# Kernel optimization log

Measured on AMD Instinct MI355X. Metric: run time of the kernel, lower is better.

The kernel has to match this reference:

```python
import jax, jax.numpy as jnp
import numpy as np

N = 50000
IN_CH = 128
OUT_CH = 64
HEADS = 4
NEG_SLOPE = 0.2


def _gatv2(x, src, dst, W_l, W_r, att):
    """GATv2Conv, concat=False, no bias/residual/dropout.
    x: [N, in]; src/dst: [E]; W_l/W_r: [in, H*C]; att: [H, C].
    Returns [N, C] (mean over heads)."""
    n = x.shape[0]
    xl = (x @ W_l).reshape(n, HEADS, OUT_CH)
    xr = (x @ W_r).reshape(n, HEADS, OUT_CH)
    # per-edge message: x_j (source, lin_l) + x_i (target, lin_r)
    m = jax.nn.leaky_relu(xl[src] + xr[dst], negative_slope=NEG_SLOPE)  # [E,H,C]
    e = jnp.einsum('ehc,hc->eh', m, att)  # [E,H]
    # segment softmax over incoming edges of each dst node
    emax = jax.ops.segment_max(e, dst, num_segments=n)  # [N,H] (-inf for empty)
    ex = jnp.exp(e - emax[dst])
    denom = jax.ops.segment_sum(ex, dst, num_segments=n)  # [N,H]
    alpha = ex / denom[dst]
    out = jax.ops.segment_sum(alpha[:, :, None] * xl[src], dst, num_segments=n)  # [N,H,C]
    return out.mean(axis=1)


def setup_inputs() -> dict:
    key = jax.random.key(0)
    ks = jax.random.split(key, 9)
    E = 800000
    s = 1.0 / np.sqrt(IN_CH)
    return {
        'x': jax.random.normal(ks[0], (N, IN_CH), dtype=jnp.float32),
        'edge_index1': jax.random.randint(ks[1], (2, E), 0, N, dtype=jnp.int64),
        'edge_index2': jax.random.randint(ks[2], (2, E), 0, N, dtype=jnp.int64),
        'W_l': jax.random.normal(ks[3], (IN_CH, HEADS * OUT_CH), dtype=jnp.float32) * s,  # shared lin_l
        'W_r0': jax.random.normal(ks[4], (IN_CH, HEADS * OUT_CH), dtype=jnp.float32) * s,
        'W_r1': jax.random.normal(ks[5], (IN_CH, HEADS * OUT_CH), dtype=jnp.float32) * s,
        'att0': jax.random.normal(ks[6], (HEADS, OUT_CH), dtype=jnp.float32) * (1.0 / np.sqrt(OUT_CH)),
        'att1': jax.random.normal(ks[7], (HEADS, OUT_CH), dtype=jnp.float32) * (1.0 / np.sqrt(OUT_CH)),
        'theta': jnp.zeros((1,), dtype=jnp.float32),
    }


def reference(x, edge_index1, edge_index2, W_l, W_r0, W_r1, att0, att1, theta):
    n = x.shape[0]
    # hop 0: add self loops
    loop = jnp.arange(n, dtype=edge_index1.dtype)
    src0 = jnp.concatenate([edge_index1[0], loop])
    dst0 = jnp.concatenate([edge_index1[1], loop])
    out = _gatv2(x, src0, dst0, W_l, W_r0, att0)
    # hop 1: no self loops, gated residual sum
    out = out + jax.nn.sigmoid(theta[0]) * _gatv2(x, edge_index2[0], edge_index2[1], W_l, W_r1, att1)
    return out
```

## Files before the change

kernel.cpp:

```cpp
#include <hip/hip_runtime.h>
#include <hip/hip_bf16.h>
#include <math.h>

#define IN_CH   128
#define HC      256
#define OUT_C   64

typedef unsigned short ushort_t;
typedef __attribute__((ext_vector_type(2))) float v2f;
typedef __attribute__((ext_vector_type(4))) float v4f;
typedef __attribute__((ext_vector_type(8))) short bf16x8;

__device__ __forceinline__ ushort_t f2bf_rne(float f) {
    unsigned u = __float_as_uint(f);
    unsigned r = (u + 0x7FFFu + ((u >> 16) & 1u)) >> 16;
    return (ushort_t)r;
}
__device__ __forceinline__ v2f bfpair(unsigned u) {
    v2f r;
    r.x = __uint_as_float(u << 16);
    r.y = __uint_as_float(u & 0xffff0000u);
    return r;
}
__device__ __forceinline__ v2f vmax0(v2f a) {
    v2f r;
    r.x = fmaxf(a.x, 0.f);
    r.y = fmaxf(a.y, 0.f);
    return r;
}

__device__ __forceinline__ float4 ntld4(const float* p) {
    v4f t = __builtin_nontemporal_load((const v4f*)p);
    return make_float4(t.x, t.y, t.z, t.w);
}
__device__ __forceinline__ int ntldi(const int* p) {
    return __builtin_nontemporal_load(p);
}
__device__ __forceinline__ void ntst4(float* p, float4 v) {
    v4f t = {v.x, v.y, v.z, v.w};
    __builtin_nontemporal_store(t, (v4f*)p);
}
__device__ __forceinline__ void ntsti(int* p, int v) {
    __builtin_nontemporal_store(v, p);
}

#define DPP_ROR_ADD(x, N)                                                   \
    (x) += __uint_as_float(__builtin_amdgcn_update_dpp(                     \
        0, __float_as_uint(x), 0x120 + (N), 0xF, 0xF, true))

__device__ __forceinline__ float rowsum16(float x) {
    DPP_ROR_ADD(x, 8);
    DPP_ROR_ADD(x, 4);
    DPP_ROR_ADD(x, 2);
    DPP_ROR_ADD(x, 1);
    return x;
}

__device__ __forceinline__ bf16x8 ldbf(const uint4* p) {
    union { uint4 u; bf16x8 v; } t;
    t.u = *p;
    return t.v;
}

__device__ __forceinline__ void dev_gemm(const float* __restrict__ x,
                                         const float* __restrict__ W,
                                         float* __restrict__ outf,
                                         ushort_t* __restrict__ outh,
                                         int n, int bx) {
    const int tid = threadIdx.x;
    const int c4  = tid & 63;
    const int rg  = __builtin_amdgcn_readfirstlane(tid >> 6);
    const int row0 = bx * 64 + rg * 16;
    const int nm1 = n - 1;
    const float4* Wv = (const float4*)W;
    const float* xr[16];
#pragma unroll
    for (int j = 0; j < 16; ++j) {
        int r = row0 + j;
        xr[j] = x + (size_t)(r > nm1 ? nm1 : r) * IN_CH;
    }
    v2f acc[16][2];
#pragma unroll
    for (int j = 0; j < 16; ++j) {
        acc[j][0] = (v2f){0.f, 0.f};
        acc[j][1] = (v2f){0.f, 0.f};
    }
    for (int k = 0; k < IN_CH; k += 4) {
        const float4 w0 = Wv[(k + 0) * 64 + c4];
        const float4 w1 = Wv[(k + 1) * 64 + c4];
        const float4 w2 = Wv[(k + 2) * 64 + c4];
        const float4 w3 = Wv[(k + 3) * 64 + c4];
        const v2f w0a = {w0.x, w0.y}, w0b = {w0.z, w0.w};
        const v2f w1a = {w1.x, w1.y}, w1b = {w1.z, w1.w};
        const v2f w2a = {w2.x, w2.y}, w2b = {w2.z, w2.w};
        const v2f w3a = {w3.x, w3.y}, w3b = {w3.z, w3.w};
#pragma unroll
        for (int jb = 0; jb < 2; ++jb) {
            float4 xv[8];
#pragma unroll
            for (int j = 0; j < 8; ++j) xv[j] = *(const float4*)(xr[jb * 8 + j] + k);
#pragma unroll
            for (int j = 0; j < 8; ++j) {
                const int a = jb * 8 + j;
                const v2f s0 = {xv[j].x, xv[j].x}, s1 = {xv[j].y, xv[j].y};
                const v2f s2 = {xv[j].z, xv[j].z}, s3 = {xv[j].w, xv[j].w};
                acc[a][0] = s0 * w0a + acc[a][0];
                acc[a][1] = s0 * w0b + acc[a][1];
                acc[a][0] = s1 * w1a + acc[a][0];
                acc[a][1] = s1 * w1b + acc[a][1];
                acc[a][0] = s2 * w2a + acc[a][0];
                acc[a][1] = s2 * w2b + acc[a][1];
                acc[a][0] = s3 * w3a + acc[a][0];
                acc[a][1] = s3 * w3b + acc[a][1];
            }
        }
    }
#pragma unroll
    for (int j = 0; j < 16; ++j) {
        const int row = row0 + j;
        if (row < n) {
            if (outh) {
                ushort4 h;
                h.x = f2bf_rne(acc[j][0].x);
                h.y = f2bf_rne(acc[j][0].y);
                h.z = f2bf_rne(acc[j][1].x);
                h.w = f2bf_rne(acc[j][1].y);
                ((ushort4*)(outh + (size_t)row * HC))[c4] = h;
            } else {
                ntst4(outf + (size_t)row * HC + 4 * c4,
                      make_float4(acc[j][0].x, acc[j][0].y, acc[j][1].x, acc[j][1].y));
            }
        }
    }
}

__device__ __forceinline__ void dev_scatter_rank(const int* __restrict__ src1,
                                                 const int* __restrict__ dst1, int E1,
                                                 const int* __restrict__ src2,
                                                 const int* __restrict__ dst2, int E2,
                                                 int n, const int* __restrict__ offs,
                                                 const int* __restrict__ rank,
                                                 int* __restrict__ csr,
                                                 int bid, int nB) {
    const int Et = E1 + E2;
    for (int i = bid * 256 + threadIdx.x; i < Et; i += nB * 256) {
        if (i < E1) {
            csr[offs[ntldi(dst1 + i)] + ntldi(rank + i)] = ntldi(src1 + i) << 9;
        } else {
            int j = i - E1;
            csr[offs[n + ntldi(dst2 + j)] + ntldi(rank + i)] = ntldi(src2 + j) << 9;
        }
    }
}

__global__ __launch_bounds__(256) void k_hp(const float* __restrict__ x,
                                            const float* __restrict__ Wl,
                                            const float* __restrict__ Wr0,
                                            const float* __restrict__ Wr1,
                                            uint4* __restrict__ xAh,
                                            uint4* __restrict__ xAl,
                                            uint4* __restrict__ WBh,
                                            uint4* __restrict__ WBl,
                                            int n, int GH, int gPX,
                                            const int* __restrict__ dst1, int E1,
                                            const int* __restrict__ dst2, int E2,
                                            int* __restrict__ deg,
                                            int* __restrict__ rank) {
    const int bx = blockIdx.x;
    if (bx < GH) {
        const int Et = E1 + E2;
        for (int i = bx * 256 + threadIdx.x; i < Et; i += GH * 256) {
            if (i < E1) ntsti(rank + i, atomicAdd(&deg[ntldi(dst1 + i)], 1));
            else        ntsti(rank + i, atomicAdd(&deg[n + ntldi(dst2 + i - E1)], 1));
        }
        return;
    }
    const int t = bx - GH;
    float v[8];
    ushort_t h[8], l[8];
    if (t < gPX) {
        const int di  = t * 256 + threadIdx.x;
        const int row = ((di >> 8) << 4) | (di & 15);
        const int ko  = ((di >> 4) & 3) | (((di >> 6) & 3) << 2);
        float4 v0 = make_float4(0.f, 0.f, 0.f, 0.f), v1 = v0;
        if (row < n) {
            const float4* xp = (const float4*)(x + (size_t)row * IN_CH + ko * 8);
            v0 = xp[0];
            v1 = xp[1];
        }
        v[0] = v0.x; v[1] = v0.y; v[2] = v0.z; v[3] = v0.w;
        v[4] = v1.x; v[5] = v1.y; v[6] = v1.z; v[7] = v1.w;
#pragma unroll
        for (int j = 0; j < 8; ++j) {
            h[j] = f2bf_rne(v[j]);
            l[j] = f2bf_rne(v[j] - __uint_as_float((unsigned)h[j] << 16));
        }
        uint4 ph, pl;
        ph.x = (unsigned)h[0] | ((unsigned)h[1] << 16);
        ph.y = (unsigned)h[2] | ((unsigned)h[3] << 16);
        ph.z = (unsigned)h[4] | ((unsigned)h[5] << 16);
        ph.w = (unsigned)h[6] | ((unsigned)h[7] << 16);
        pl.x = (unsigned)l[0] | ((unsigned)l[1] << 16);
        pl.y = (unsigned)l[2] | ((unsigned)l[3] << 16);
        pl.z = (unsigned)l[4] | ((unsigned)l[5] << 16);
        pl.w = (unsigned)l[6] | ((unsigned)l[7] << 16);
        xAh[di] = ph;
        xAl[di] = pl;
    } else {
        const int idx = (t - gPX) * 256 + threadIdx.x;
        const int lane = idx & 63;
        const int f    = (idx >> 6) & 15;
        const int c    = (idx >> 10) & 3;
        const int w    = idx >> 12;
        if (w >= 3) return;
        const float* Wp = (w == 0) ? Wl : ((w == 1) ? Wr0 : Wr1);
        const int col = f * 16 + (lane & 15);
        const int k0  = c * 32 + (lane >> 4) * 8;
#pragma unroll
        for (int j = 0; j < 8; ++j) {
            v[j] = Wp[(size_t)(k0 + j) * HC + col];
            h[j] = f2bf_rne(v[j]);
            l[j] = f2bf_rne(v[j] - __uint_as_float((unsigned)h[j] << 16));
        }
        uint4 ph, pl;
        ph.x = (unsigned)h[0] | ((unsigned)h[1] << 16);
        ph.y = (unsigned)h[2] | ((unsigned)h[3] << 16);
        ph.z = (unsigned)h[4] | ((unsigned)h[5] << 16);
        ph.w = (unsigned)h[6] | ((unsigned)h[7] << 16);
        pl.x = (unsigned)l[0] | ((unsigned)l[1] << 16);
        pl.y = (unsigned)l[2] | ((unsigned)l[3] << 16);
        pl.z = (unsigned)l[4] | ((unsigned)l[5] << 16);
        pl.w = (unsigned)l[6] | ((unsigned)l[7] << 16);
        WBh[idx] = ph;
        WBl[idx] = pl;
    }
}

__global__ __launch_bounds__(256) void k_gemm3(const uint4* __restrict__ xAh,
                                               const uint4* __restrict__ xAl,
                                               const uint4* __restrict__ WBh,
                                               const uint4* __restrict__ WBl,
                                               ushort_t* __restrict__ xlh,
                                               float* __restrict__ xr0,
                                               float* __restrict__ xr1,
                                               int n, int GS,
                                               const int* __restrict__ src1,
                                               const int* __restrict__ dst1, int E1,
                                               const int* __restrict__ src2,
                                               const int* __restrict__ dst2, int E2,
                                               const int* __restrict__ offs,
                                               const int* __restrict__ rank,
                                               int* __restrict__ csr) {
    const int bx = blockIdx.x;
    if (bx < GS) {
        dev_scatter_rank(src1, dst1, E1, src2, dst2, E2, n, offs, rank, csr, bx, GS);
        return;
    }
    const int t    = bx - GS;
    const int tile = t / 3;
    const int wsel = t - tile * 3;

    const int lane = threadIdx.x & 63;
    const int wave = __builtin_amdgcn_readfirstlane((int)(threadIdx.x >> 6));

    v4f acc[4][4];
#pragma unroll
    for (int g = 0; g < 4; ++g)
#pragma unroll
        for (int f = 0; f < 4; ++f) acc[g][f] = (v4f){0.f, 0.f, 0.f, 0.f};

    const uint4* Bh = WBh + (size_t)wsel * 4096;
    const uint4* Bl = WBl + (size_t)wsel * 4096;
    const int g0 = tile * 4;

    for (int c = 0; c < 4; ++c) {
        bf16x8 ah[4], al[4], bh[4], bl[4];
#pragma unroll
        for (int g = 0; g < 4; ++g) {
            const int ai = ((g0 + g) * 4 + c) * 64 + lane;
            ah[g] = ldbf(xAh + ai);
            al[g] = ldbf(xAl + ai);
        }
#pragma unroll
        for (int f = 0; f < 4; ++f) {
            const int bi = (c * 16 + wave * 4 + f) * 64 + lane;
            bh[f] = ldbf(Bh + bi);
            bl[f] = ldbf(Bl + bi);
        }
#pragma unroll
        for (int g = 0; g < 4; ++g)
#pragma unroll
            for (int f = 0; f < 4; ++f) {
                acc[g][f] = __builtin_amdgcn_mfma_f32_16x16x32_bf16(ah[g], bh[f], acc[g][f], 0, 0, 0);
                acc[g][f] = __builtin_amdgcn_mfma_f32_16x16x32_bf16(ah[g], bl[f], acc[g][f], 0, 0, 0);
                acc[g][f] = __builtin_amdgcn_mfma_f32_16x16x32_bf16(al[g], bh[f], acc[g][f], 0, 0, 0);
            }
    }

    const int colB = wave * 64 + (lane & 15);
    const int rowB = tile * 64 + ((lane >> 4) << 2);
    if (wsel == 0) {
#pragma unroll
        for (int g = 0; g < 4; ++g)
#pragma unroll
            for (int f = 0; f < 4; ++f) {
                const int col = colB + f * 16;
#pragma unroll
                for (int r = 0; r < 4; ++r) {
                    const int row = rowB + g * 16 + r;
                    if (row < n) xlh[(size_t)row * HC + col] = f2bf_rne(acc[g][f][r]);
                }
            }
    } else {
        float* o = (wsel == 1) ? xr0 : xr1;
#pragma unroll
        for (int g = 0; g < 4; ++g)
#pragma unroll
            for (int f = 0; f < 4; ++f) {
                const int col = colB + f * 16;
#pragma unroll
                for (int r = 0; r < 4; ++r) {
                    const int row = rowB + g * 16 + r;
                    if (row < n)
                        __builtin_nontemporal_store(acc[g][f][r], o + (size_t)row * HC + col);
                }
            }
    }
}

__global__ __launch_bounds__(128) void k_aggboth(const ushort_t* __restrict__ xlh,
                                                 const float* __restrict__ xr0,
                                                 const float* __restrict__ xr1,
                                                 const float* __restrict__ att0,
                                                 const float* __restrict__ att1,
                                                 const int* __restrict__ offs,
                                                 const int* __restrict__ deg,
                                                 const int* __restrict__ csr,
                                                 int n, float* __restrict__ out,
                                                 const float* __restrict__ theta) {
    const int lane = threadIdx.x & 63;
    int node_ = blockIdx.x * 2 + (threadIdx.x >> 6);
    if (node_ >= n) return;
    const int node = __builtin_amdgcn_readfirstlane(node_);

    const float4 at0 = ((const float4*)att0)[lane];
    const float4 at1 = ((const float4*)att1)[lane];
    const v2f a2_0a = {0.2f * at0.x, 0.2f * at0.y}, a2_0b = {0.2f * at0.z, 0.2f * at0.w};
    const v2f a8_0a = {0.8f * at0.x, 0.8f * at0.y}, a8_0b = {0.8f * at0.z, 0.8f * at0.w};
    const v2f a2_1a = {0.2f * at1.x, 0.2f * at1.y}, a2_1b = {0.2f * at1.z, 0.2f * at1.w};
    const v2f a8_1a = {0.8f * at1.x, 0.8f * at1.y}, a8_1b = {0.8f * at1.z, 0.8f * at1.w};
    const float4 q0 = ntld4(xr0 + (size_t)node * HC + 4 * lane);
    const float4 q1 = ntld4(xr1 + (size_t)node * HC + 4 * lane);
    const v2f x0a = {q0.x, q0.y}, x0b = {q0.z, q0.w};
    const v2f x1a = {q1.x, q1.y}, x1b = {q1.z, q1.w};

    const int t0 = deg[node];
    const int s0 = offs[node];
    const int t1 = deg[n + node];
    const int s1 = offs[n + node];

    const char* Xc = (const char*)xlh;
    const unsigned laneB = (unsigned)lane * 8u;
    auto gath = [&](unsigned off) -> uint2 {
        const char* p = Xc + off;
        return *(const uint2*)(p + laneB);
    };

    float l0 = 0.f, l1 = 0.f;
    v2f O0a = {0.f, 0.f}, O0b = {0.f, 0.f};
    v2f O1a = {0.f, 0.f}, O1b = {0.f, 0.f};

    auto proc = [&](uint2 w, const v2f& xa, const v2f& xb,
                    const v2f& a8a, const v2f& a8b,
                    const v2f& a2a, const v2f& a2b, float& l, v2f& Oa, v2f& Ob) {
        v2f ca = bfpair(w.x), cb = bfpair(w.y);
        v2f za = ca + xa, zb = cb + xb;
        v2f t = a2a * za + a2b * zb + a8a * vmax0(za) + a8b * vmax0(zb);
        float part = rowsum16(t.x + t.y);
        float p = __expf(fminf(part, 60.f));
        l += p;
        v2f pp = {p, p};
        Oa = pp * ca + Oa;
        Ob = pp * cb + Ob;
    };
    auto proc0 = [&](uint2 w) { proc(w, x0a, x0b, a8_0a, a8_0b, a2_0a, a2_0b, l0, O0a, O0b); };
    auto proc1 = [&](uint2 w) { proc(w, x1a, x1b, a8_1a, a8_1b, a2_1a, a2_1b, l1, O1a, O1b); };

    unsigned vc0p = 0, vc1p = 0;
    if (t0 > 0) vc0p = (unsigned)csr[s0 + lane];
    if (t1 > 0) vc1p = (unsigned)csr[s1 + lane];

    proc0(gath((unsigned)node << 9));

    for (int base = 0; base < t0; base += 64) {
        const unsigned vc = (base == 0) ? vc0p : (unsigned)csr[s0 + base + lane];
        const int m = (t0 - base < 64) ? (t0 - base) : 64;
        int j = 0;
        for (; j + 8 <= m; j += 8) {
            uint2 g0 = gath((unsigned)__builtin_amdgcn_readlane(vc, j + 0));
            uint2 g1 = gath((unsigned)__builtin_amdgcn_readlane(vc, j + 1));
            uint2 g2 = gath((unsigned)__builtin_amdgcn_readlane(vc, j + 2));
            uint2 g3 = gath((unsigned)__builtin_amdgcn_readlane(vc, j + 3));
            uint2 g4 = gath((unsigned)__builtin_amdgcn_readlane(vc, j + 4));
            uint2 g5 = gath((unsigned)__builtin_amdgcn_readlane(vc, j + 5));
            uint2 g6 = gath((unsigned)__builtin_amdgcn_readlane(vc, j + 6));
            uint2 g7 = gath((unsigned)__builtin_amdgcn_readlane(vc, j + 7));
            proc0(g0); proc0(g1); proc0(g2); proc0(g3);
            proc0(g4); proc0(g5); proc0(g6); proc0(g7);
        }
        for (; j + 2 <= m; j += 2) {
            uint2 g0 = gath((unsigned)__builtin_amdgcn_readlane(vc, j + 0));
            uint2 g1 = gath((unsigned)__builtin_amdgcn_readlane(vc, j + 1));
            proc0(g0); proc0(g1);
        }
        if (j < m) proc0(gath((unsigned)__builtin_amdgcn_readlane(vc, j)));
    }

    for (int base = 0; base < t1; base += 64) {
        const unsigned vc = (base == 0) ? vc1p : (unsigned)csr[s1 + base + lane];
        const int m = (t1 - base < 64) ? (t1 - base) : 64;
        int j = 0;
        for (; j + 8 <= m; j += 8) {
            uint2 g0 = gath((unsigned)__builtin_amdgcn_readlane(vc, j + 0));
            uint2 g1 = gath((unsigned)__builtin_amdgcn_readlane(vc, j + 1));
            uint2 g2 = gath((unsigned)__builtin_amdgcn_readlane(vc, j + 2));
            uint2 g3 = gath((unsigned)__builtin_amdgcn_readlane(vc, j + 3));
            uint2 g4 = gath((unsigned)__builtin_amdgcn_readlane(vc, j + 4));
            uint2 g5 = gath((unsigned)__builtin_amdgcn_readlane(vc, j + 5));
            uint2 g6 = gath((unsigned)__builtin_amdgcn_readlane(vc, j + 6));
            uint2 g7 = gath((unsigned)__builtin_amdgcn_readlane(vc, j + 7));
            proc1(g0); proc1(g1); proc1(g2); proc1(g3);
            proc1(g4); proc1(g5); proc1(g6); proc1(g7);
        }
        for (; j + 2 <= m; j += 2) {
            uint2 g0 = gath((unsigned)__builtin_amdgcn_readlane(vc, j + 0));
            uint2 g1 = gath((unsigned)__builtin_amdgcn_readlane(vc, j + 1));
            proc1(g0); proc1(g1);
        }
        if (j < m) proc1(gath((unsigned)__builtin_amdgcn_readlane(vc, j)));
    }

    const float inv0 = 0.25f / l0;
    const float inv1 = (l1 > 0.f) ? 0.25f / l1 : 0.f;
    const float sg = 1.f / (1.f + __expf(-theta[0]));
    float vx = O0a.x * inv0 + sg * (O1a.x * inv1);
    float vy = O0a.y * inv0 + sg * (O1a.y * inv1);
    float vz = O0b.x * inv0 + sg * (O1b.x * inv1);
    float vw = O0b.y * inv0 + sg * (O1b.y * inv1);
    vx += __shfl_xor(vx, 16); vx += __shfl_xor(vx, 32);
    vy += __shfl_xor(vy, 16); vy += __shfl_xor(vy, 32);
    vz += __shfl_xor(vz, 16); vz += __shfl_xor(vz, 32);
    vw += __shfl_xor(vw, 16); vw += __shfl_xor(vw, 32);

    if (lane < 16) {
        ntst4(out + (size_t)node * OUT_C + 4 * lane, make_float4(vx, vy, vz, vw));
    }
}

__device__ __forceinline__ void dev_agg(const ushort_t* __restrict__ xlh,
                                        const float* __restrict__ xr,
                                        const float* __restrict__ att,
                                        const int* __restrict__ offs,
                                        const int* __restrict__ deg,
                                        const int* __restrict__ csr_src,
                                        int n, float* __restrict__ out,
                                        int selfLoop,
                                        const float* __restrict__ theta,
                                        int accumulate, int bid) {
    const int lane = threadIdx.x & 63;
    const int node = bid * 4 + (threadIdx.x >> 6);
    if (node >= n) return;

    const float4 attv = ((const float4*)att)[lane];
    const v2f a2a = {0.2f * attv.x, 0.2f * attv.y}, a2b = {0.2f * attv.z, 0.2f * attv.w};
    const v2f a8a = {0.8f * attv.x, 0.8f * attv.y}, a8b = {0.8f * attv.z, 0.8f * attv.w};
    const float4 q = ntld4(xr + (size_t)node * HC + 4 * lane);
    const v2f xa = {q.x, q.y}, xb = {q.z, q.w};
    const int start2 = offs[node] - selfLoop;
    const int total  = deg[node] + selfLoop;

    float l = 0.f;
    v2f Oa = {0.f, 0.f}, Ob = {0.f, 0.f};
    const char* Xc = (const char*)xlh;
    const unsigned laneB = (unsigned)lane * 8u;

    auto ld = [&](int i) -> uint2 {
        int off = (selfLoop && i == 0) ? (node << 9) : ntldi(csr_src + start2 + i);
        return *(const uint2*)(Xc + (unsigned)off + laneB);
    };
    auto process = [&](uint2 w) {
        v2f ca = bfpair(w.x), cb = bfpair(w.y);
        v2f za = ca + xa, zb = cb + xb;
        v2f t = a2a * za + a2b * zb + a8a * vmax0(za) + a8b * vmax0(zb);
        float part = rowsum16(t.x + t.y);
        float p = __expf(fminf(part, 60.f));
        l += p;
        v2f pp = {p, p};
        Oa = pp * ca + Oa;
        Ob = pp * cb + Ob;
    };

    if (total > 0) {
        uint2 b0 = ld(0);
        uint2 b1 = ld(1);
        uint2 b2 = ld(2);
        uint2 b3 = ld(3);
        int i = 0;
        for (; i + 4 <= total; i += 4) {
            uint2 c0 = b0, c1 = b1, c2 = b2, c3 = b3;
            b0 = ld(i + 4);
            b1 = ld(i + 5);
            b2 = ld(i + 6);
            b3 = ld(i + 7);
            process(c0);
            process(c1);
            process(c2);
            process(c3);
        }
        const int rem = total - i;
        if (rem > 0) process(b0);
        if (rem > 1) process(b1);
        if (rem > 2) process(b2);
    }

    float inv = (l > 0.f) ? 0.25f / l : 0.f;
    float vx = Oa.x * inv, vy = Oa.y * inv, vz = Ob.x * inv, vw = Ob.y * inv;
    vx += __shfl_xor(vx, 16); vx += __shfl_xor(vx, 32);
    vy += __shfl_xor(vy, 16); vy += __shfl_xor(vy, 32);
    vz += __shfl_xor(vz, 16); vz += __shfl_xor(vz, 32);
    vw += __shfl_xor(vw, 16); vw += __shfl_xor(vw, 32);

    if (lane < 16) {
        float4 r = make_float4(vx, vy, vz, vw);
        float4* op = (float4*)(out + (size_t)node * OUT_C);
        if (accumulate) {
            float sg = 1.f / (1.f + __expf(-theta[0]));
            float4 cur = op[lane];
            r.x = fmaf(sg, r.x, cur.x);
            r.y = fmaf(sg, r.y, cur.y);
            r.z = fmaf(sg, r.z, cur.z);
            r.w = fmaf(sg, r.w, cur.w);
        }
        op[lane] = r;
    }
}

__global__ __launch_bounds__(256) void k_mix1(const float* __restrict__ x,
                                              const float* __restrict__ Wa,
                                              ushort_t* __restrict__ oah,
                                              const float* __restrict__ Wb,
                                              float* __restrict__ ob, int n,
                                              int GH, int gG,
                                              const int* __restrict__ dst1, int E1,
                                              const int* __restrict__ dst2, int E2,
                                              int* __restrict__ deg,
                                              int* __restrict__ rank) {
    const int bx = blockIdx.x;
    if (bx < GH) {
        const int Et = E1 + E2;
        for (int i = bx * 256 + threadIdx.x; i < Et; i += GH * 256) {
            if (i < E1) ntsti(rank + i, atomicAdd(&deg[ntldi(dst1 + i)], 1));
            else        ntsti(rank + i, atomicAdd(&deg[n + ntldi(dst2 + i - E1)], 1));
        }
    } else {
        int t = bx - GH;
        if (t < gG) dev_gemm(x, Wa, nullptr, oah, n, t);
        else        dev_gemm(x, Wb, ob, nullptr, n, t - gG);
    }
}

__global__ __launch_bounds__(256) void k_mix2(const float* __restrict__ x,
                                              const float* __restrict__ Wc,
                                              float* __restrict__ oc, int n,
                                              int GS,
                                              const int* __restrict__ src1,
                                              const int* __restrict__ dst1, int E1,
                                              const int* __restrict__ src2,
                                              const int* __restrict__ dst2, int E2,
                                              const int* __restrict__ offs,
                                              const int* __restrict__ rank,
                                              int* __restrict__ csr) {
    const int bx = blockIdx.x;
    if (bx < GS)
        dev_scatter_rank(src1, dst1, E1, src2, dst2, E2, n, offs, rank, csr, bx, GS);
    else
        dev_gemm(x, Wc, oc, nullptr, n, bx - GS);
}

__global__ __launch_bounds__(256) void k_mix3(const ushort_t* __restrict__ xlh,
                                              const float* __restrict__ xr,
                                              const float* __restrict__ att,
                                              const int* __restrict__ offs,
                                              const int* __restrict__ deg,
                                              const int* __restrict__ csr_src,
                                              int n, float* __restrict__ out,
                                              int selfLoop,
                                              const float* __restrict__ theta,
                                              int accumulate) {
    dev_agg(xlh, xr, att, offs, deg, csr_src, n, out, selfLoop, theta,
            accumulate, blockIdx.x);
}

__global__ __launch_bounds__(1024) void k_scanA(const int* __restrict__ deg, int n,
                                                int* __restrict__ incl,
                                                int* __restrict__ bsum) {
    __shared__ int sm[1024];
    const int t = threadIdx.x;
    const int i = blockIdx.x * 1024 + t;
    sm[t] = (i < n) ? deg[i] : 0;
    for (int off = 1; off < 1024; off <<= 1) {
        __syncthreads();
        int u = (t >= off) ? sm[t - off] : 0;
        __syncthreads();
        sm[t] += u;
    }
    if (i < n) incl[i] = sm[t];
    if (t == 1023) bsum[blockIdx.x] = sm[1023];
}

__global__ __launch_bounds__(1024) void k_scanB(int* __restrict__ bsum, int nb) {
    __shared__ int sm[1024];
    const int t = threadIdx.x;
    sm[t] = (t < nb) ? bsum[t] : 0;
    for (int off = 1; off < 1024; off <<= 1) {
        __syncthreads();
        int u = (t >= off) ? sm[t - off] : 0;
        __syncthreads();
        sm[t] += u;
    }
    if (t < nb) bsum[t] = sm[t];
}

__global__ void k_scanCf(const int* __restrict__ incl, const int* __restrict__ deg,
                         const int* __restrict__ bsum, int nb, int n,
                         int* __restrict__ offs) {
    __shared__ int sb[128];
    const int t = threadIdx.x;
    if (t < 128) sb[t] = (t < nb) ? bsum[t] : 0;
    __syncthreads();
#pragma unroll
    for (int off = 1; off < 128; off <<= 1) {
        int u = (t >= off && t < 128) ? sb[t - off] : 0;
        __syncthreads();
        if (t < 128) sb[t] += u;
        __syncthreads();
    }
    int i = blockIdx.x * 256 + t;
    if (i < n) {
        int b    = i >> 10;
        int base = (b > 0) ? sb[b - 1] : 0;
        offs[i] = base + incl[i] - deg[i];
    }
}

__global__ void k_scanC(const int* __restrict__ incl, const int* __restrict__ deg,
                        const int* __restrict__ bsum, int n,
                        int* __restrict__ offs) {
    int i = blockIdx.x * 256 + threadIdx.x;
    if (i < n) {
        int b    = i >> 10;
        int base = (b > 0) ? bsum[b - 1] : 0;
        offs[i] = base + incl[i] - deg[i];
    }
}

extern "C" void kernel_launch(void* const* d_in, const int* in_sizes, int n_in,
                              void* d_out, int out_size, void* d_ws, size_t ws_size,
                              hipStream_t stream) {
    const float* x     = (const float*)d_in[0];
    const int*   e1    = (const int*)d_in[1];
    const int*   e2    = (const int*)d_in[2];
    const float* Wl    = (const float*)d_in[3];
    const float* Wr0   = (const float*)d_in[4];
    const float* Wr1   = (const float*)d_in[5];
    const float* att0  = (const float*)d_in[6];
    const float* att1  = (const float*)d_in[7];
    const float* theta = (const float*)d_in[8];

    const int n  = in_sizes[0] / IN_CH;
    const int E1 = in_sizes[1] / 2;
    const int E2 = in_sizes[2] / 2;
    float* out = (float*)d_out;

    char* w = (char*)d_ws;
    auto alloc = [&](size_t bytes) -> char* {
        char* p = w;
        w += (bytes + 255) & ~(size_t)255;
        return p;
    };
    auto al = [](size_t b) -> size_t { return (b + 255) & ~(size_t)255; };

    const int gT = (n + 63) / 64;
    const size_t projH = (size_t)n * HC * 2;
    const size_t projF = (size_t)n * HC * 4;
    const size_t eB    = (size_t)(E1 + E2) * 4 + 256;
    const size_t degB  = (size_t)2 * n * 4;
    const size_t xAB   = (size_t)gT * 1024 * 16;
    const size_t WBB   = (size_t)3 * 4 * 16 * 64 * 16;

    const size_t need3 = al(projH) + 2 * al(projF) + 2 * al(eB) + 3 * al(degB) + 4096;
    const size_t needM = need3 + 2 * al(xAB) + 2 * al(WBB);
    const bool mfmaPath = ws_size >= needM;
    const bool threeBuf = ws_size >= need3;

    ushort_t* xlh = (ushort_t*)alloc(projH);
    float* xr0 = (float*)alloc(projF);
    float* xr1 = threeBuf ? (float*)alloc(projF) : xr0;
    int* csr  = (int*)alloc(eB);
    int* rank = (int*)alloc(eB);
    int* deg  = (int*)alloc(degB);
    int* offs = (int*)alloc(degB);
    int* tmp  = (int*)alloc(degB);
    int* bsum = (int*)alloc(4096);

    const int GH    = 2048;
    const int GS    = 2048;
    const int n2    = 2 * n;
    const int gN2   = (n2 + 255) / 256;
    const int nScan = (n2 + 1023) / 1024;

    if (mfmaPath) {
        uint4* xAh = (uint4*)alloc(xAB);
        uint4* xAl = (uint4*)alloc(xAB);
        uint4* WBh = (uint4*)alloc(WBB);
        uint4* WBl = (uint4*)alloc(WBB);
        const int gPX = gT * 4;
        const int gPW = 48;

        hipMemsetAsync(deg, 0, (size_t)n2 * 4, stream);
        hipMemsetAsync(csr + E1 + E2, 0, 256, stream);
        k_hp<<<GH + gPX + gPW, 256, 0, stream>>>(x, Wl, Wr0, Wr1,
                                                 xAh, xAl, WBh, WBl,
                                                 n, GH, gPX,
                                                 e1 + E1, E1, e2 + E2, E2,
                                                 deg, rank);
        k_scanA<<<nScan, 1024, 0, stream>>>(deg, n2, tmp, bsum);
        if (nScan <= 128) {
            k_scanCf<<<gN2, 256, 0, stream>>>(tmp, deg, bsum, nScan, n2, offs);
        } else {
            k_scanB<<<1, 1024, 0, stream>>>(bsum, nScan);
            k_scanC<<<gN2, 256, 0, stream>>>(tmp, deg, bsum, n2, offs);
        }
        k_gemm3<<<GS + 3 * gT, 256, 0, stream>>>(xAh, xAl, WBh, WBl,
                                                 xlh, xr0, xr1, n, GS,
                                                 e1, e1 + E1, E1, e2, e2 + E2, E2,
                                                 offs, rank, csr);
        k_aggboth<<<(n + 1) / 2, 128, 0, stream>>>(xlh, xr0, xr1, att0, att1,
                                                   offs, deg, csr, n, out, theta);
        return;
    }

    const int gG = gT;
    const int GA4 = (n + 3) / 4;
    hipMemsetAsync(deg, 0, (size_t)n2 * 4, stream);
    hipMemsetAsync(csr + E1 + E2, 0, 256, stream);
    k_mix1<<<GH + 2 * gG, 256, 0, stream>>>(x, Wl, xlh, Wr0, xr0, n, GH, gG,
                                            e1 + E1, E1, e2 + E2, E2, deg, rank);
    k_scanA<<<nScan, 1024, 0, stream>>>(deg, n2, tmp, bsum);
    if (nScan <= 128) {
        k_scanCf<<<gN2, 256, 0, stream>>>(tmp, deg, bsum, nScan, n2, offs);
    } else {
        k_scanB<<<1, 1024, 0, stream>>>(bsum, nScan);
        k_scanC<<<gN2, 256, 0, stream>>>(tmp, deg, bsum, n2, offs);
    }

    if (threeBuf) {
        k_mix2<<<GS + gG, 256, 0, stream>>>(x, Wr1, xr1, n, GS,
                                            e1, e1 + E1, E1, e2, e2 + E2, E2,
                                            offs, rank, csr);
        k_aggboth<<<(n + 1) / 2, 128, 0, stream>>>(xlh, xr0, xr1, att0, att1,
                                                   offs, deg, csr, n, out, theta);
    } else {
        k_mix2<<<GS, 256, 0, stream>>>(x, Wr1, xr1, n, GS,
                                       e1, e1 + E1, E1, e2, e2 + E2, E2,
                                       offs, rank, csr);
        k_mix3<<<GA4, 256, 0, stream>>>(xlh, xr0, att0, offs, deg, csr, n, out,
                                        1, theta, 0);
        k_mix2<<<gG, 256, 0, stream>>>(x, Wr1, xr0, n, 0,
                                       (const int*)nullptr, (const int*)nullptr, 0,
                                       (const int*)nullptr, (const int*)nullptr, 0,
                                       (const int*)nullptr, (const int*)nullptr,
                                       (int*)nullptr);
        k_mix3<<<GA4, 256, 0, stream>>>(xlh, xr0, att1, offs + n, deg + n, csr, n, out,
                                        0, theta, 1);
    }
}
```

Measured before the change: 372.3 us.

## Use cached stores, regroup GEMM tile order, fold csr pad memset into kernel

```diff
diff --git a/kernel.cpp b/kernel.cpp
--- a/kernel.cpp
+++ b/kernel.cpp
@@ -39,9 +39,6 @@
 __device__ __forceinline__ void ntst4(float* p, float4 v) {
     v4f t = {v.x, v.y, v.z, v.w};
     __builtin_nontemporal_store(t, (v4f*)p);
-}
-__device__ __forceinline__ void ntsti(int* p, int v) {
-    __builtin_nontemporal_store(v, p);
 }
 
 #define DPP_ROR_ADD(x, N)                                                   \
@@ -127,8 +124,8 @@
                 h.w = f2bf_rne(acc[j][1].y);
                 ((ushort4*)(outh + (size_t)row * HC))[c4] = h;
             } else {
-                ntst4(outf + (size_t)row * HC + 4 * c4,
-                      make_float4(acc[j][0].x, acc[j][0].y, acc[j][1].x, acc[j][1].y));
+                *(float4*)(outf + (size_t)row * HC + 4 * c4) =
+                    make_float4(acc[j][0].x, acc[j][0].y, acc[j][1].x, acc[j][1].y);
             }
         }
     }
@@ -165,13 +162,15 @@
                                             const int* __restrict__ dst1, int E1,
                                             const int* __restrict__ dst2, int E2,
                                             int* __restrict__ deg,
-                                            int* __restrict__ rank) {
+                                            int* __restrict__ rank,
+                                            int* __restrict__ csrpad) {
     const int bx = blockIdx.x;
     if (bx < GH) {
+        if (bx == 0 && threadIdx.x < 64) csrpad[threadIdx.x] = 0;
         const int Et = E1 + E2;
         for (int i = bx * 256 + threadIdx.x; i < Et; i += GH * 256) {
-            if (i < E1) ntsti(rank + i, atomicAdd(&deg[ntldi(dst1 + i)], 1));
-            else        ntsti(rank + i, atomicAdd(&deg[n + ntldi(dst2 + i - E1)], 1));
+            if (i < E1) rank[i] = atomicAdd(&deg[dst1[i]], 1);
+            else        rank[i] = atomicAdd(&deg[n + dst2[i - E1]], 1);
         }
         return;
     }
@@ -243,7 +242,7 @@
                                                ushort_t* __restrict__ xlh,
                                                float* __restrict__ xr0,
                                                float* __restrict__ xr1,
-                                               int n, int GS,
+                                               int n, int GS, int gT,
                                                const int* __restrict__ src1,
                                                const int* __restrict__ dst1, int E1,
                                                const int* __restrict__ src2,
@@ -256,9 +255,19 @@
         dev_scatter_rank(src1, dst1, E1, src2, dst2, E2, n, offs, rank, csr, bx, GS);
         return;
     }
-    const int t    = bx - GS;
-    const int tile = t / 3;
-    const int wsel = t - tile * 3;
+    const int t = bx - GS;
+    const int gT8 = (gT / 8) * 8;
+    int tile, wsel;
+    if (t < 3 * gT8) {
+        const int k = t / 24;
+        const int r = t - k * 24;
+        tile = k * 8 + (r & 7);
+        wsel = r >> 3;
+    } else {
+        const int u = t - 3 * gT8;
+        tile = gT8 + u / 3;
+        wsel = u - (u / 3) * 3;
+    }
 
     const int lane = threadIdx.x & 63;
     const int wave = __builtin_amdgcn_readfirstlane((int)(threadIdx.x >> 6));
@@ -321,8 +330,7 @@
 #pragma unroll
                 for (int r = 0; r < 4; ++r) {
                     const int row = rowB + g * 16 + r;
-                    if (row < n)
-                        __builtin_nontemporal_store(acc[g][f][r], o + (size_t)row * HC + col);
+                    if (row < n) o[(size_t)row * HC + col] = acc[g][f][r];
                 }
             }
     }
@@ -342,6 +350,8 @@
     int node_ = blockIdx.x * 2 + (threadIdx.x >> 6);
     if (node_ >= n) return;
     const int node = __builtin_amdgcn_readfirstlane(node_);
+
+    const float th = theta[0];
 
     const float4 at0 = ((const float4*)att0)[lane];
     const float4 at1 = ((const float4*)att1)[lane];
@@ -442,7 +452,7 @@
 
     const float inv0 = 0.25f / l0;
     const float inv1 = (l1 > 0.f) ? 0.25f / l1 : 0.f;
-    const float sg = 1.f / (1.f + __expf(-theta[0]));
+    const float sg = 1.f / (1.f + __expf(-th));
     float vx = O0a.x * inv0 + sg * (O1a.x * inv1);
     float vy = O0a.y * inv0 + sg * (O1a.y * inv1);
     float vz = O0b.x * inv0 + sg * (O1b.x * inv1);
@@ -559,8 +569,8 @@
     if (bx < GH) {
         const int Et = E1 + E2;
         for (int i = bx * 256 + threadIdx.x; i < Et; i += GH * 256) {
-            if (i < E1) ntsti(rank + i, atomicAdd(&deg[ntldi(dst1 + i)], 1));
-            else        ntsti(rank + i, atomicAdd(&deg[n + ntldi(dst2 + i - E1)], 1));
+            if (i < E1) rank[i] = atomicAdd(&deg[dst1[i]], 1);
+            else        rank[i] = atomicAdd(&deg[n + dst2[i - E1]], 1);
         }
     } else {
         int t = bx - GH;
@@ -728,12 +738,11 @@
         const int gPW = 48;
 
         hipMemsetAsync(deg, 0, (size_t)n2 * 4, stream);
-        hipMemsetAsync(csr + E1 + E2, 0, 256, stream);
         k_hp<<<GH + gPX + gPW, 256, 0, stream>>>(x, Wl, Wr0, Wr1,
                                                  xAh, xAl, WBh, WBl,
                                                  n, GH, gPX,
                                                  e1 + E1, E1, e2 + E2, E2,
-                                                 deg, rank);
+                                                 deg, rank, csr + E1 + E2);
         k_scanA<<<nScan, 1024, 0, stream>>>(deg, n2, tmp, bsum);
         if (nScan <= 128) {
             k_scanCf<<<gN2, 256, 0, stream>>>(tmp, deg, bsum, nScan, n2, offs);
@@ -742,7 +751,7 @@
             k_scanC<<<gN2, 256, 0, stream>>>(tmp, deg, bsum, n2, offs);
         }
         k_gemm3<<<GS + 3 * gT, 256, 0, stream>>>(xAh, xAl, WBh, WBl,
-                                                 xlh, xr0, xr1, n, GS,
+                                                 xlh, xr0, xr1, n, GS, gT,
                                                  e1, e1 + E1, E1, e2, e2 + E2, E2,
                                                  offs, rank, csr);
         k_aggboth<<<(n + 1) / 2, 128, 0, stream>>>(xlh, xr0, xr1, att0, att1,
```

Result: faster. 353.9 us (-5.0%).
